# Kernel optimization log

Hardware: AMD Instinct MI355X
Metric: run time of the kernel (lower is better)

## Reference

```python
import jax, jax.numpy as jnp
import numpy as np

KHS = 3        # kernel_half_size
SIGMA = 1.6    # sigma / dx
DX = 1.0
C = 20.0       # accumulate() hard-codes c = 20


def _gauss_kernel():
    size = 2 * KHS + 1
    g = np.arange(size, dtype=np.float32) - (size - 1) / 2.0
    g = np.exp(-(g / SIGMA) ** 2 / 2.0) / (SIGMA * np.sqrt(2.0 * np.pi))
    k = g[:, None, None] * g[None, :, None] * g[None, None, :]
    k = k / k.sum()
    return jnp.asarray(k[None, None], dtype=jnp.float32)  # [1,1,7,7,7]


def _smooth(x, kernel):
    # depthwise (single-channel) 3d gaussian conv, 'same' padding, zero bias
    return jax.lax.conv_general_dilated(
        x, kernel, window_strides=(1, 1, 1),
        padding=[(KHS, KHS)] * 3,
        dimension_numbers=("NCDHW", "OIDHW", "NCDHW"))


def _fdiff(f, axis):
    # forward difference, replicate last difference to keep size (torchJacobian3 style)
    d = jnp.diff(f, axis=axis)
    last = jax.lax.slice_in_dim(d, d.shape[axis] - 1, d.shape[axis], axis=axis)
    return jnp.concatenate([d, last], axis=axis)


def _curl(v):
    # v: [B,3,D,H,W]; per-channel fields are [B,D,H,W]; z->axis1, y->axis2, x->axis3
    u, vv, w = v[:, 0], v[:, 1], v[:, 2]
    cu = _fdiff(w, 2) - _fdiff(vv, 1)   # dw/dy - dv/dz
    cv = _fdiff(u, 1) - _fdiff(w, 3)    # du/dz - dw/dx
    cw = _fdiff(vv, 3) - _fdiff(u, 2)   # dv/dx - du/dy
    return jnp.stack([cu, cv, cw], axis=1)


def _integrate(t, v):
    # trapezoidal transmittance-weighted integral along depth (dim 2)
    front = (1.0 - t[:, :, 0]) * v[:, :, 0]
    trap = jnp.sum((t[:, :, :-1] - t[:, :, 1:]) * (v[:, :, :-1] + v[:, :, 1:]) * 0.5, axis=2)
    return front + trap


def setup_inputs() -> dict:
    key = jax.random.key(0)
    k1, k2 = jax.random.split(key)
    d = jax.random.uniform(k1, (4, 1, 128, 128, 128), dtype=jnp.float32)
    v = jax.random.normal(k2, (4, 3, 128, 128, 128), dtype=jnp.float32)
    return {"d": d, "v": v}


def reference(d, v):
    kern = _gauss_kernel()
    ds = _smooth(d, kern)
    vort = _curl(v) / DX
    vn = jnp.sqrt(jnp.sum(vort ** 2, axis=1, keepdims=True))  # [B,1,D,H,W]
    vn = _smooth(vn, kern)
    # single default view dir 'zp' -> identity rotation
    df = jnp.flip(ds, axis=2)
    vf = jnp.flip(vn, axis=2)
    x = jnp.cumsum(df * DX, axis=2)
    t = (x * C + 1.0) * jnp.exp(-C * x)
    iv = _integrate(t, vf)              # [B,1,H,W]
    return jnp.clip(iv, 0.0, 1.0)
```

## Files before the change

kernel.cpp:

```cpp
#include <hip/hip_runtime.h>
#include <math.h>

#define NB 4
#define DD 128
#define HH 128
#define WW 128
#define VOX (DD*HH*WW)
#define NVOX (NB*VOX)

struct GaussW { float w[7]; };

__device__ __forceinline__ float4 f4zero() { float4 z; z.x = z.y = z.z = z.w = 0.f; return z; }

__device__ __forceinline__ float4 curl4_at(const float* __restrict__ u,
                                           const float* __restrict__ vv,
                                           const float* __restrict__ w,
                                           int z, int y, int x0) {
    int xq = x0 >> 2;
    size_t s = ((size_t)z << 14) | ((size_t)y << 7) | (size_t)x0;
    int dy = (y < 127) ? 128 : -128;
    int dz = (z < 127) ? 16384 : -16384;
    float sy = (y < 127) ? 1.f : -1.f;
    float sz = (z < 127) ? 1.f : -1.f;
    int dxp = (xq < 31) ? 4 : 0;

    const float4 wc  = *(const float4*)(w  + s);
    const float4 wyn = *(const float4*)(w  + s + dy);
    const float4 vc  = *(const float4*)(vv + s);
    const float4 vzn = *(const float4*)(vv + s + dz);
    const float4 uc  = *(const float4*)(u  + s);
    const float4 uzn = *(const float4*)(u  + s + dz);
    const float4 uyn = *(const float4*)(u  + s + dy);
    const float  wxp = w [s + 3 + dxp];
    const float  vxp = vv[s + 3 + dxp];

    float wca[4] = {wc.x, wc.y, wc.z, wc.w};
    float vca[4] = {vc.x, vc.y, vc.z, vc.w};
    float wya[4] = {wyn.x, wyn.y, wyn.z, wyn.w};
    float vza[4] = {vzn.x, vzn.y, vzn.z, vzn.w};
    float uca[4] = {uc.x, uc.y, uc.z, uc.w};
    float uza[4] = {uzn.x, uzn.y, uzn.z, uzn.w};
    float uya[4] = {uyn.x, uyn.y, uyn.z, uyn.w};
    float wsh[4] = {wc.y, wc.z, wc.w, wxp};
    float vsh[4] = {vc.y, vc.z, vc.w, vxp};

    float4 o;
    float* oa = &o.x;
#pragma unroll
    for (int j = 0; j < 4; ++j) {
        int x = x0 + j;
        float fdxw = (x < 127) ? (wsh[j] - wca[j]) : (wca[3] - wca[2]);
        float fdxv = (x < 127) ? (vsh[j] - vca[j]) : (vca[3] - vca[2]);
        float fdyw = sy * (wya[j] - wca[j]);
        float fdyu = sy * (uya[j] - uca[j]);
        float fdzv = sz * (vza[j] - vca[j]);
        float fdzu = sz * (uza[j] - uca[j]);
        float cu = fdyw - fdzv;
        float cv = fdzu - fdxw;
        float cw = fdxv - fdyu;
        oa[j] = sqrtf(cu * cu + cv * cv + cw * cw);
    }
    return o;
}

__global__ __launch_bounds__(256, 4)
void yx_curl_dual_kernel(const float* __restrict__ dIn, float* __restrict__ P,
                         const float* __restrict__ v,   float* __restrict__ Q,
                         GaussW gw) {
    __shared__ float in_t[38][128];
    __shared__ float mid[32][136];

    int bb = blockIdx.x;
    bool isCurl = (bb >= 2048);
    int b  = bb & 2047;
    int yq = b & 3;
    int z  = (b >> 2) & 127;
    int n  = b >> 9;
    int y0 = yq * 32;
    size_t slice = (((size_t)n << 7) | (size_t)z) << 14;
    int tid = threadIdx.x;

    if (!isCurl) {
        for (int j = tid; j < 38 * 32; j += 256) {
            int r  = j >> 5;
            int c4 = (j & 31) << 2;
            int gy = y0 - 3 + r;
            float4 val = (gy >= 0 && gy < 128)
                       ? *(const float4*)(dIn + slice + ((size_t)gy << 7) + c4)
                       : f4zero();
            *(float4*)&in_t[r][c4] = val;
        }
    } else {
        const float* u  = v + (size_t)n * 3 * VOX;
        const float* vv = u + VOX;
        const float* w  = vv + VOX;
        for (int j = tid; j < 38 * 32; j += 256) {
            int r  = j >> 5;
            int c4 = (j & 31) << 2;
            int gy = y0 - 3 + r;
            float4 val = (gy >= 0 && gy < 128)
                       ? curl4_at(u, vv, w, z, gy, c4)
                       : f4zero();
            *(float4*)&in_t[r][c4] = val;
        }
    }
    __syncthreads();

    if (tid < 32) {
        *(float4*)&mid[tid][0]   = f4zero();
        *(float4*)&mid[tid][132] = f4zero();
    }
    for (int j = tid; j < 32 * 32; j += 256) {
        int yo = j >> 5;
        int c4 = (j & 31) << 2;
        float4 a = f4zero();
#pragma unroll
        for (int k = 0; k < 7; ++k) {
            float wk = gw.w[k];
            float4 t = *(const float4*)&in_t[yo + k][c4];
            a.x += wk * t.x; a.y += wk * t.y; a.z += wk * t.z; a.w += wk * t.w;
        }
        *(float4*)&mid[yo][c4 + 4] = a;
    }
    __syncthreads();

    float* out = isCurl ? Q : P;
    for (int j = tid; j < 32 * 32; j += 256) {
        int yo  = j >> 5;
        int x0c = (j & 31) << 2;
        float4 m0 = *(const float4*)&mid[yo][x0c];
        float4 m1 = *(const float4*)&mid[yo][x0c + 4];
        float4 m2 = *(const float4*)&mid[yo][x0c + 8];
        float wdw[12] = {m0.x, m0.y, m0.z, m0.w,
                         m1.x, m1.y, m1.z, m1.w,
                         m2.x, m2.y, m2.z, m2.w};
        float o[4];
#pragma unroll
        for (int j2 = 0; j2 < 4; ++j2) {
            float acc = 0.f;
#pragma unroll
            for (int k = 0; k < 7; ++k) acc += gw.w[k] * wdw[j2 + 1 + k];
            o[j2] = acc;
        }
        *(float4*)(out + slice + ((size_t)(y0 + yo) << 7) + x0c) =
            make_float4(o[0], o[1], o[2], o[3]);
    }
}

#define RBATCH 16
__global__ __launch_bounds__(256, 2)
void render_zs_kernel(const float* __restrict__ P, const float* __restrict__ Q,
                      float* __restrict__ out, GaussW gw) {
    int idx = blockIdx.x * blockDim.x + threadIdx.x;
    if (idx >= NB * HH * WW) return;
    int x = idx & 127;
    int y = (idx >> 7) & 127;
    int n = idx >> 14;
    size_t volbase = (size_t)n * VOX + ((size_t)y << 7) + x;

    float pc[6], qc[6];
#pragma unroll
    for (int t = 0; t < 3; ++t) { pc[t] = 0.f; qc[t] = 0.f; }
#pragma unroll
    for (int t = 3; t < 6; ++t) {
        int j = t - 3;
        size_t off = volbase + ((size_t)(127 - j) << 14);
        pc[t] = P[off];
        qc[t] = Q[off];
    }

    float xacc = 0.f, acc = 0.f, tp = 0.f, vp = 0.f;
    for (int b = 0; b < 128 / RBATCH; ++b) {
        int j0 = b * RBATCH;
        float pw[RBATCH + 6], qw[RBATCH + 6];
#pragma unroll
        for (int t = 0; t < 6; ++t) { pw[t] = pc[t]; qw[t] = qc[t]; }
#pragma unroll
        for (int i = 0; i < RBATCH; ++i) {
            int j = j0 + 3 + i;
            if (j <= 127) {
                size_t off = volbase + ((size_t)(127 - j) << 14);
                pw[6 + i] = P[off];
                qw[6 + i] = Q[off];
            } else {
                pw[6 + i] = 0.f;
                qw[6 + i] = 0.f;
            }
        }
#pragma unroll
        for (int i = 0; i < RBATCH; ++i) {
            float dsf = 0.f, vnf = 0.f;
#pragma unroll
            for (int k = 0; k < 7; ++k) {
                float wk = gw.w[k];
                dsf += wk * pw[i + k];
                vnf += wk * qw[i + k];
            }
            xacc += dsf;
            float xc = 20.f * xacc;
            float tk = (xc + 1.f) * __expf(-xc);
            if (j0 + i == 0) acc = (1.f - tk) * vnf;
            else             acc += (tp - tk) * (vp + vnf) * 0.5f;
            tp = tk; vp = vnf;
        }
#pragma unroll
        for (int t = 0; t < 6; ++t) { pc[t] = pw[RBATCH + t]; qc[t] = qw[RBATCH + t]; }
    }
    out[idx] = fminf(fmaxf(acc, 0.f), 1.f);
}

extern "C" void kernel_launch(void* const* d_in, const int* in_sizes, int n_in,
                              void* d_out, int out_size, void* d_ws, size_t ws_size,
                              hipStream_t stream) {
    const float* d = (const float*)d_in[0];
    const float* v = (const float*)d_in[1];
    float* out = (float*)d_out;

    GaussW gw;
    {
        double g[7], s = 0.0;
        for (int i = 0; i < 7; ++i) {
            double t = (i - 3) / 1.6;
            g[i] = exp(-t * t / 2.0);
            s += g[i];
        }
        for (int i = 0; i < 7; ++i) gw.w[i] = (float)(g[i] / s);
    }

    float* ws0 = (float*)d_ws;
    float* ws1 = ws0 + NVOX;

    const int TB = 256;

    yx_curl_dual_kernel<<<2 * NB * DD * 4, TB, 0, stream>>>(d, ws0, v, ws1, gw);

    render_zs_kernel<<<(NB * HH * WW) / TB, TB, 0, stream>>>(ws0, ws1, out, gw);
}
```

Before: 202.8 us.

## Split depth render into four chunks per column and drop mid LDS buffer

The render kernel previously gave each column to one thread, which walked all 128 depth slices in sequence, so only 256 blocks were launched. It now splits each column into four 32-slice chunks handled by separate threads, and combines them through shared-memory prefix sums of the density and partial integrals, launching four times as many threads. In the yx smoothing kernel, the separate mid shared buffer is removed: the y-pass results are held in registers and written back into in_t, cutting shared memory so more blocks can be resident. The cost is larger register arrays, which may cause spills, plus an extra barrier in each kernel.

New measurement: 198.2 us. 1.02x faster.

```diff
diff --git a/kernel.cpp b/kernel.cpp
--- a/kernel.cpp
+++ b/kernel.cpp
@@ -68,7 +68,6 @@
                          const float* __restrict__ v,   float* __restrict__ Q,
                          GaussW gw) {
     __shared__ float in_t[38][128];
-    __shared__ float mid[32][136];
 
     int bb = blockIdx.x;
     bool isCurl = (bb >= 2048);
@@ -106,40 +105,50 @@
     }
     __syncthreads();
 
-    if (tid < 32) {
-        *(float4*)&mid[tid][0]   = f4zero();
-        *(float4*)&mid[tid][132] = f4zero();
-    }
-    for (int j = tid; j < 32 * 32; j += 256) {
+    float4 rr[4];
+#pragma unroll
+    for (int t = 0; t < 4; ++t) {
+        int j  = tid + t * 256;
         int yo = j >> 5;
         int c4 = (j & 31) << 2;
         float4 a = f4zero();
 #pragma unroll
         for (int k = 0; k < 7; ++k) {
             float wk = gw.w[k];
-            float4 t = *(const float4*)&in_t[yo + k][c4];
-            a.x += wk * t.x; a.y += wk * t.y; a.z += wk * t.z; a.w += wk * t.w;
-        }
-        *(float4*)&mid[yo][c4 + 4] = a;
+            float4 tv = *(const float4*)&in_t[yo + k][c4];
+            a.x += wk * tv.x; a.y += wk * tv.y; a.z += wk * tv.z; a.w += wk * tv.w;
+        }
+        rr[t] = a;
+    }
+    __syncthreads();
+
+#pragma unroll
+    for (int t = 0; t < 4; ++t) {
+        int j  = tid + t * 256;
+        int yo = j >> 5;
+        int c4 = (j & 31) << 2;
+        *(float4*)&in_t[yo][c4] = rr[t];
     }
     __syncthreads();
 
     float* out = isCurl ? Q : P;
-    for (int j = tid; j < 32 * 32; j += 256) {
+#pragma unroll
+    for (int t = 0; t < 4; ++t) {
+        int j   = tid + t * 256;
         int yo  = j >> 5;
         int x0c = (j & 31) << 2;
-        float4 m0 = *(const float4*)&mid[yo][x0c];
-        float4 m1 = *(const float4*)&mid[yo][x0c + 4];
-        float4 m2 = *(const float4*)&mid[yo][x0c + 8];
-        float wdw[12] = {m0.x, m0.y, m0.z, m0.w,
-                         m1.x, m1.y, m1.z, m1.w,
-                         m2.x, m2.y, m2.z, m2.w};
+        float4 q0 = (x0c > 0)   ? *(const float4*)&in_t[yo][x0c - 4] : f4zero();
+        float4 q1 =               *(const float4*)&in_t[yo][x0c];
+        float4 q2 = (x0c < 124) ? *(const float4*)&in_t[yo][x0c + 4] : f4zero();
+        float wdw[11] = {q0.y, q0.z, q0.w,
+                         q1.x, q1.y, q1.z, q1.w,
+                         q2.x, q2.y, q2.z, q2.w};
         float o[4];
 #pragma unroll
         for (int j2 = 0; j2 < 4; ++j2) {
             float acc = 0.f;
 #pragma unroll
-            for (int k = 0; k < 7; ++k) acc += gw.w[k] * wdw[j2 + 1 + k];
+            for (int k = 0; k < 7; ++k) acc += gw.w[k] * wdw[j2 + k];
             o[j2] = acc;
         }
         *(float4*)(out + slice + ((size_t)(y0 + yo) << 7) + x0c) =
@@ -147,66 +156,80 @@
     }
 }
 
-#define RBATCH 16
-__global__ __launch_bounds__(256, 2)
-void render_zs_kernel(const float* __restrict__ P, const float* __restrict__ Q,
-                      float* __restrict__ out, GaussW gw) {
-    int idx = blockIdx.x * blockDim.x + threadIdx.x;
-    if (idx >= NB * HH * WW) return;
-    int x = idx & 127;
-    int y = (idx >> 7) & 127;
-    int n = idx >> 14;
-    size_t volbase = (size_t)n * VOX + ((size_t)y << 7) + x;
-
-    float pc[6], qc[6];
-#pragma unroll
-    for (int t = 0; t < 3; ++t) { pc[t] = 0.f; qc[t] = 0.f; }
-#pragma unroll
-    for (int t = 3; t < 6; ++t) {
-        int j = t - 3;
-        size_t off = volbase + ((size_t)(127 - j) << 14);
-        pc[t] = P[off];
-        qc[t] = Q[off];
-    }
-
-    float xacc = 0.f, acc = 0.f, tp = 0.f, vp = 0.f;
-    for (int b = 0; b < 128 / RBATCH; ++b) {
-        int j0 = b * RBATCH;
-        float pw[RBATCH + 6], qw[RBATCH + 6];
-#pragma unroll
-        for (int t = 0; t < 6; ++t) { pw[t] = pc[t]; qw[t] = qc[t]; }
-#pragma unroll
-        for (int i = 0; i < RBATCH; ++i) {
-            int j = j0 + 3 + i;
-            if (j <= 127) {
-                size_t off = volbase + ((size_t)(127 - j) << 14);
-                pw[6 + i] = P[off];
-                qw[6 + i] = Q[off];
-            } else {
-                pw[6 + i] = 0.f;
-                qw[6 + i] = 0.f;
-            }
-        }
-#pragma unroll
-        for (int i = 0; i < RBATCH; ++i) {
-            float dsf = 0.f, vnf = 0.f;
-#pragma unroll
-            for (int k = 0; k < 7; ++k) {
-                float wk = gw.w[k];
-                dsf += wk * pw[i + k];
-                vnf += wk * qw[i + k];
-            }
-            xacc += dsf;
-            float xc = 20.f * xacc;
-            float tk = (xc + 1.f) * __expf(-xc);
-            if (j0 + i == 0) acc = (1.f - tk) * vnf;
-            else             acc += (tp - tk) * (vp + vnf) * 0.5f;
-            tp = tk; vp = vnf;
-        }
-#pragma unroll
-        for (int t = 0; t < 6; ++t) { pc[t] = pw[RBATCH + t]; qc[t] = qw[RBATCH + t]; }
-    }
-    out[idx] = fminf(fmaxf(acc, 0.f), 1.f);
+__global__ __launch_bounds__(256, 4)
+void render_zs4_kernel(const float* __restrict__ P, const float* __restrict__ Q,
+                       float* __restrict__ out, GaussW gw) {
+    __shared__ float csum[4][64];
+    __shared__ float part[4][64];
+
+    int xl = threadIdx.x & 63;
+    int ch = threadIdx.x >> 6;
+    int col = blockIdx.x * 64 + xl;
+    int x = col & 127;
+    int y = (col >> 7) & 127;
+    int n = col >> 14;
+    size_t volbase = ((size_t)n << 21) | ((size_t)y << 7) | (size_t)x;
+    int j0 = ch * 32;
+
+    float a[38];
+#pragma unroll
+    for (int t = 0; t < 38; ++t) {
+        int j = j0 - 3 + t;
+        a[t] = (j >= 0 && j <= 127) ? P[volbase + ((size_t)(127 - j) << 14)] : 0.f;
+    }
+#pragma unroll
+    for (int i = 0; i < 32; ++i) {
+        float s = 0.f;
+#pragma unroll
+        for (int k = 0; k < 7; ++k) s += gw.w[k] * a[i + k];
+        a[i] = s;
+    }
+    float S = 0.f;
+#pragma unroll
+    for (int i = 0; i < 32; ++i) S += a[i];
+    csum[ch][xl] = S;
+
+    float bq[39];
+#pragma unroll
+    for (int t = 0; t < 39; ++t) {
+        int j = j0 - 4 + t;
+        bq[t] = (j >= 0 && j <= 127) ? Q[volbase + ((size_t)(127 - j) << 14)] : 0.f;
+    }
+    __syncthreads();
+
+    float offset = 0.f;
+    if (ch > 0) offset += csum[0][xl];
+    if (ch > 1) offset += csum[1][xl];
+    if (ch > 2) offset += csum[2][xl];
+
+    float tp = 0.f, vp = 0.f, acc = 0.f, xacc = offset;
+    if (ch > 0) {
+        float v0 = 0.f;
+#pragma unroll
+        for (int k = 0; k < 7; ++k) v0 += gw.w[k] * bq[k];
+        vp = v0;
+        float xc = 20.f * offset;
+        tp = (xc + 1.f) * __expf(-xc);
+    }
+#pragma unroll
+    for (int i = 0; i < 32; ++i) {
+        xacc += a[i];
+        float vk = 0.f;
+#pragma unroll
+        for (int k = 0; k < 7; ++k) vk += gw.w[k] * bq[i + 1 + k];
+        float xc = 20.f * xacc;
+        float tk = (xc + 1.f) * __expf(-xc);
+        if (ch == 0 && i == 0) acc = (1.f - tk) * vk;
+        else                   acc += (tp - tk) * (vp + vk) * 0.5f;
+        tp = tk; vp = vk;
+    }
+    part[ch][xl] = acc;
+    __syncthreads();
+
+    if (ch == 0) {
+        float r = part[0][xl] + part[1][xl] + part[2][xl] + part[3][xl];
+        out[col] = fminf(fmaxf(r, 0.f), 1.f);
+    }
 }
 
 extern "C" void kernel_launch(void* const* d_in, const int* in_sizes, int n_in,
@@ -234,5 +257,5 @@
 
     yx_curl_dual_kernel<<<2 * NB * DD * 4, TB, 0, stream>>>(d, ws0, v, ws1, gw);
 
-    render_zs_kernel<<<(NB * HH * WW) / TB, TB, 0, stream>>>(ws0, ws1, out, gw);
-}
+    render_zs4_kernel<<<(NB * HH * WW) / 64, TB, 0, stream>>>(ws0, ws1, out, gw);
+}
```
